# Performance work log

Hardware: AMD Instinct MI355X
Metric: run time of the kernel (lower is better)

## Reference

```python
import math
import jax, jax.numpy as jnp
import numpy as np

B, S, D, H = 8, 512, 1024, 16
DH = D // H
NEG_BIG = -1.0e30  # stands in for torch's -np.inf (exp underflows to 0 identically)


def setup_inputs() -> dict:
    key0 = jax.random.key(0)
    ks = jax.random.split(key0, 20)
    n = lambda k, shp, s=1.0: jax.random.normal(k, shp, dtype=jnp.float32) * s
    inp = {}
    inp["query"] = n(ks[0], (B, S, D))
    inp["key"] = n(ks[1], (B, S, D))
    inp["value"] = n(ks[2], (B, S, D))
    # rel has exact zeros (they get masked to -10000 before its softmax)
    inp["rel"] = jax.random.randint(ks[3], (B, S, S), 0, 3).astype(jnp.float32)
    inp["timestamp"] = n(ks[4], (B, S, S))
    inp["l1"] = jnp.float32(0.3)
    inp["l2"] = jnp.float32(0.3)
    # causal mask: True = masked (future positions)
    inp["mask"] = jnp.broadcast_to(jnp.triu(jnp.ones((S, S), dtype=bool), k=1), (B, S, S))
    inp["encode_pos"] = 0
    # three qkv projection linears (total_size -> total_size)
    w = 1.0 / math.sqrt(D)
    inp["Wq"], inp["bq"] = n(ks[5], (D, D), w), jnp.zeros((D,), jnp.float32)
    inp["Wk"], inp["bk"] = n(ks[6], (D, D), w), jnp.zeros((D,), jnp.float32)
    inp["Wv"], inp["bv"] = n(ks[7], (D, D), w), jnp.zeros((D,), jnp.float32)
    # clip_factor / guessing_factor: Linear(head_size -> 1) applied to per-head key
    wh = 1.0 / math.sqrt(DH)
    inp["Wc"], inp["bc"] = n(ks[8], (1, DH), wh), jnp.zeros((1,), jnp.float32)
    inp["Wg"], inp["bg"] = n(ks[9], (1, DH), wh), jnp.zeros((1,), jnp.float32)
    return inp


def reference(query, key, value, rel, timestamp, l1, l2, mask, encode_pos,
              Wq, bq, Wk, bk, Wv, bv, Wc, bc, Wg, bg):
    b, s, d = query.shape
    dh = Wc.shape[1]
    h = d // dh

    def proj(x, W, bias):  # [b,s,d] -> [b,h,s,dh]
        return (x @ W.T + bias).reshape(b, s, h, dh).transpose(0, 2, 1, 3)

    q = proj(query, Wq, bq)
    k = proj(key, Wk, bk)
    v = proj(value, Wv, bv)

    m4 = mask[:, None]          # [b,1,s,s] broadcast over heads
    rel4 = rel[:, None]         # [b,1,s,s]
    ts4 = timestamp[:, None]    # [b,1,s,s]

    # relative softmax: zeros masked to -10000
    rel_attn = jax.nn.softmax(jnp.where(rel4 == 0, -10000.0, rel4), axis=-1)

    # scaled dot-product scores
    scores = jnp.einsum('bhqd,bhkd->bhqk', q, k) / math.sqrt(dh)
    scores = jnp.where(m4, -1.0e9, scores)

    # clip / guessing factors from per-head key -> [b,h,s,1]
    cf = k @ Wc.T + bc
    gf = k @ Wg.T + bg
    R1 = jax.nn.sigmoid(gf - cf) + gf

    # time-decay softmax
    time_stamp = jnp.where(m4, NEG_BIG, jnp.exp(-jnp.abs(ts4)))
    Rs = time_stamp + R1  # [b,h,s,s] (R1 broadcasts over last axis, as in torch)

    prob_attn = jax.nn.softmax(scores, axis=-1)
    time_attn = jax.nn.softmax(Rs, axis=-1)
    prob_attn = (1.0 - l2) * prob_attn + l2 * time_attn
    prob_attn = (1.0 - l1) * prob_attn + l1 * rel_attn

    out = jnp.einsum('bhqk,bhkd->bhqd', prob_attn, v)
    out = out.transpose(0, 2, 1, 3).reshape(b, s, d)
    return out, prob_attn
```

## Files before the change

kernel.cpp:

```cpp
#include <hip/hip_runtime.h>
#include <math.h>

typedef __attribute__((ext_vector_type(8))) short short8;
typedef __attribute__((ext_vector_type(4))) float f32x4;

#define B_  8
#define S_  512
#define D_  1024
#define H_  16
#define DH_ 64

__device__ __forceinline__ unsigned short f2bf(float f) {
    unsigned int u = __float_as_uint(f);
    u += 0x7FFFu + ((u >> 16) & 1u);
    return (unsigned short)(u >> 16);
}
__device__ __forceinline__ float bf2f(unsigned short u) {
    return __uint_as_float(((unsigned int)u) << 16);
}
__device__ __forceinline__ void gload_lds16(const void* g, void* l) {
    __builtin_amdgcn_global_load_lds(
        (const __attribute__((address_space(1))) unsigned int*)g,
        (__attribute__((address_space(3))) unsigned int*)l, 16, 0, 0);
}

__global__ __launch_bounds__(256) void conv_bf16(
    const float* __restrict__ q, const float* __restrict__ k, const float* __restrict__ v,
    const float* __restrict__ wq, const float* __restrict__ wk, const float* __restrict__ wv,
    unsigned short* __restrict__ Abf, unsigned short* __restrict__ Wbf)
{
    const size_t NA = 1048576;
    const size_t NW = 262144;
    const size_t total = 3*NA + 3*NW;
    for (size_t i4 = (size_t)blockIdx.x*blockDim.x + threadIdx.x; i4 < total;
         i4 += (size_t)gridDim.x*blockDim.x) {
        const float* s; unsigned short* d; size_t off;
        if (i4 < 3*NA) {
            const int z = (int)(i4 / NA);
            s = (z == 0) ? q : (z == 1) ? k : v;
            off = i4 - (size_t)z*NA;
            d = Abf + (size_t)z*NA*4;
        } else {
            const size_t j = i4 - 3*NA;
            const int z = (int)(j / NW);
            s = (z == 0) ? wq : (z == 1) ? wk : wv;
            off = j - (size_t)z*NW;
            d = Wbf + (size_t)z*NW*4;
        }
        const float4 f = ((const float4*)s)[off];
        ushort4 u; u.x = f2bf(f.x); u.y = f2bf(f.y); u.z = f2bf(f.z); u.w = f2bf(f.w);
        ((ushort4*)d)[off] = u;
    }
}

__global__ __launch_bounds__(256) void qkv_gemm(
    const unsigned short* __restrict__ Abf, const unsigned short* __restrict__ Wbf,
    const float* __restrict__ bq, const float* __restrict__ bk, const float* __restrict__ bv,
    unsigned short* __restrict__ qw, unsigned short* __restrict__ kw,
    unsigned short* __restrict__ vw)
{
    __shared__ unsigned short As[128][64];
    __shared__ unsigned short Bs[128][64];

    const int bid = blockIdx.x;
    const int wid = (bid & 7) * 96 + (bid >> 3);
    const int z   = wid >> 8;
    const int rem = wid & 255;
    const int bm  = (rem >> 3) * 128;
    const int bn  = (rem & 7) * 128;

    const unsigned short* A = Abf + (size_t)z * 4194304;
    const unsigned short* W = Wbf + (size_t)z * 1048576;
    const float* bias = (z == 0) ? bq : (z == 1) ? bk : bv;
    unsigned short* outp = (z == 0) ? qw : (z == 1) ? kw : vw;
    const float scale = (z == 0) ? 0.125f : 1.0f;

    const int t = threadIdx.x, w = t >> 6, l = t & 63, lr = l & 15, lg = l >> 4;
    const int wr = (w >> 1) * 64, wc = (w & 1) * 64;

    const int srow = t >> 3;
    const int scol = 8 * ((t & 7) ^ (srow & 7));
    const unsigned short* Ast = A + (size_t)(bm + srow) * 1024 + scol;
    const unsigned short* Wst = W + (size_t)(bn + srow) * 1024 + scol;
    char* AsB = (char*)As; char* BsB = (char*)Bs;

    f32x4 acc[4][4] = {};
    for (int k0 = 0; k0 < 1024; k0 += 64) {
        __syncthreads();
        #pragma unroll
        for (int j = 0; j < 4; j++) {
            gload_lds16(Ast + (size_t)(32*j)*1024 + k0, AsB + 4096*j + t*16);
            gload_lds16(Wst + (size_t)(32*j)*1024 + k0, BsB + 4096*j + t*16);
        }
        __syncthreads();
        #pragma unroll
        for (int s = 0; s < 2; s++) {
            short8 af[4], bf4[4];
            #pragma unroll
            for (int i = 0; i < 4; i++) {
                const int row = wr + 16*i + lr;
                af[i] = *(const short8*)(AsB + row*128 + (((4*s + lg) ^ (row & 7)) << 4));
            }
            #pragma unroll
            for (int j = 0; j < 4; j++) {
                const int row = wc + 16*j + lr;
                bf4[j] = *(const short8*)(BsB + row*128 + (((4*s + lg) ^ (row & 7)) << 4));
            }
            #pragma unroll
            for (int i = 0; i < 4; i++)
                #pragma unroll
                for (int j = 0; j < 4; j++)
                    acc[i][j] = __builtin_amdgcn_mfma_f32_16x16x32_bf16(af[i], bf4[j], acc[i][j], 0, 0, 0);
        }
    }

    #pragma unroll
    for (int j = 0; j < 4; j++) {
        const int n = bn + wc + 16*j + lr;
        const float bvx = bias[n];
        const int h = n >> 6, dh = n & 63;
        #pragma unroll
        for (int i = 0; i < 4; i++)
            #pragma unroll
            for (int r = 0; r < 4; r++) {
                const int m = bm + wr + 16*i + 4*lg + r;
                const int bb = m >> 9, s = m & 511;
                outp[(((size_t)(bb*H_ + h))*S_ + s)*DH_ + dh] = f2bf((acc[i][j][r] + bvx) * scale);
            }
    }
}

__global__ __launch_bounds__(256) void vtrans(const unsigned short* __restrict__ vw,
                                              unsigned short* __restrict__ vtw)
{
    __shared__ unsigned short tile[64][68];
    const int bh = blockIdx.y, sc = blockIdx.x * 64;
    const unsigned short* src = vw + (size_t)bh * S_ * DH_;
    unsigned short* dst = vtw + (size_t)bh * DH_ * S_;
    const int t = threadIdx.x;
    const int r = t >> 4, c4 = (t & 15) << 2;
    #pragma unroll
    for (int i = 0; i < 4; i++)
        *(ushort4*)&tile[r + 16*i][c4] = *(const ushort4*)&src[(size_t)(sc + r + 16*i)*DH_ + c4];
    __syncthreads();
    const int dh = t >> 2, sg = (t & 3) * 16;
    #pragma unroll
    for (int e = 0; e < 16; e += 4) {
        ushort4 u;
        u.x = tile[sg + e + 0][dh]; u.y = tile[sg + e + 1][dh];
        u.z = tile[sg + e + 2][dh]; u.w = tile[sg + e + 3][dh];
        *(ushort4*)&dst[(size_t)dh*S_ + sc + sg + e] = u;
    }
}

__global__ __launch_bounds__(256) void e_kernel(
    const float* __restrict__ rel, const float* __restrict__ tsp,
    const float* __restrict__ pl1, const float* __restrict__ pl2,
    unsigned short* __restrict__ E)
{
    const int t = threadIdx.x, w = t >> 6, l = t & 63;
    const int ridx = blockIdx.x * 4 + w;
    const int q = ridx & (S_ - 1);
    const float l1 = *pl1, l2 = *pl2;
    const float c_t = (1.f - l1) * l2, c_r = l1;
    const float* tr = tsp + (size_t)ridx * S_;
    const float* rr = rel + (size_t)ridx * S_;

    float tv[8], rv[8]; float st = 0.f, sr = 0.f;
    #pragma unroll
    for (int j = 0; j < 8; j++) {
        const int k = l + 64*j;
        const float rvv = rr[k];
        rv[j] = (rvv != 0.f) ? __expf(rvv) : 0.f;
        sr += rv[j];
        float tvv = 0.f;
        if (k <= q) tvv = __expf(__expf(-fabsf(tr[k])));
        tv[j] = tvv; st += tvv;
    }
    #pragma unroll
    for (int m = 32; m; m >>= 1) { st += __shfl_xor(st, m); sr += __shfl_xor(sr, m); }
    const float ti   = c_t / st;
    const float riv  = (sr > 0.f) ? c_r / sr : 0.f;
    const float runi = (sr > 0.f) ? 0.f : c_r / (float)S_;

    unsigned short* Er = E + (size_t)ridx * S_;
    #pragma unroll
    for (int j = 0; j < 8; j++) {
        const int k = l + 64*j;
        Er[k] = f2bf(tv[j]*ti + rv[j]*riv + runi);
    }
}

__global__ __launch_bounds__(256) void attn_mfma(
    const unsigned short* __restrict__ qw, const unsigned short* __restrict__ kw,
    const unsigned short* __restrict__ vtw, const unsigned short* __restrict__ E,
    const float* __restrict__ pl1, const float* __restrict__ pl2,
    float* __restrict__ out, float* __restrict__ prob)
{
    __shared__ unsigned short Ps[2][64][72];

    const int t = threadIdx.x, w = t >> 6, l = t & 63, lr = l & 15, lg = l >> 4;
    const int bid = blockIdx.x;
    const int j   = bid >> 3;
    const int bh  = (bid & 7) * 16 + (j & 15);
    const int b   = bh >> 4, h = bh & 15;
    const int q0  = (j >> 4) * 64;
    const float l1 = *pl1, l2 = *pl2;
    const float c_p = (1.f - l1) * (1.f - l2);
    const unsigned short* qp = qw + (size_t)bh * (S_ * DH_);
    const unsigned short* kp = kw + (size_t)bh * (S_ * DH_);
    const unsigned short* vt = vtw + (size_t)bh * (DH_ * S_);

    short8 qa[2];
    #pragma unroll
    for (int s = 0; s < 2; s++)
        qa[s] = *(const short8*)&qp[(size_t)(q0 + 16*w + lr)*DH_ + 32*s + 8*lg];

    const int qrb = q0 + 16*w + 4*lg;

    unsigned int scp[8][4][2];
    #pragma unroll
    for (int ch = 0; ch < 8; ch++) {
        f32x4 a4[4] = {};
        #pragma unroll
        for (int s = 0; s < 2; s++)
            #pragma unroll
            for (int g = 0; g < 4; g++) {
                const short8 kb = *(const short8*)&kp[(size_t)(ch*64 + 16*g + lr)*DH_ + 32*s + 8*lg];
                a4[g] = __builtin_amdgcn_mfma_f32_16x16x32_bf16(qa[s], kb, a4[g], 0, 0, 0);
            }
        #pragma unroll
        for (int g = 0; g < 4; g++) {
            const int k = 64*ch + 16*g + lr;
            const float v0 = (k <= qrb + 0) ? a4[g][0] : -1e30f;
            const float v1 = (k <= qrb + 1) ? a4[g][1] : -1e30f;
            const float v2 = (k <= qrb + 2) ? a4[g][2] : -1e30f;
            const float v3 = (k <= qrb + 3) ? a4[g][3] : -1e30f;
            scp[ch][g][0] = ((unsigned)f2bf(v1) << 16) | f2bf(v0);
            scp[ch][g][1] = ((unsigned)f2bf(v3) << 16) | f2bf(v2);
        }
    }

    float mx[4] = {-1e30f, -1e30f, -1e30f, -1e30f};
    #pragma unroll
    for (int ch = 0; ch < 8; ch++)
        #pragma unroll
        for (int g = 0; g < 4; g++) {
            const unsigned u0 = scp[ch][g][0], u1 = scp[ch][g][1];
            mx[0] = fmaxf(mx[0], __uint_as_float(u0 << 16));
            mx[1] = fmaxf(mx[1], __uint_as_float(u0 & 0xffff0000u));
            mx[2] = fmaxf(mx[2], __uint_as_float(u1 << 16));
            mx[3] = fmaxf(mx[3], __uint_as_float(u1 & 0xffff0000u));
        }
    #pragma unroll
    for (int i = 0; i < 4; i++)
        #pragma unroll
        for (int m = 8; m; m >>= 1) mx[i] = fmaxf(mx[i], __shfl_xor(mx[i], m));

    float sm[4] = {0.f, 0.f, 0.f, 0.f};
    #pragma unroll
    for (int ch = 0; ch < 8; ch++)
        #pragma unroll
        for (int g = 0; g < 4; g++) {
            const unsigned u0 = scp[ch][g][0], u1 = scp[ch][g][1];
            const float e0 = __expf(__uint_as_float(u0 << 16)          - mx[0]);
            const float e1 = __expf(__uint_as_float(u0 & 0xffff0000u) - mx[1]);
            const float e2 = __expf(__uint_as_float(u1 << 16)          - mx[2]);
            const float e3 = __expf(__uint_as_float(u1 & 0xffff0000u) - mx[3]);
            sm[0] += e0; sm[1] += e1; sm[2] += e2; sm[3] += e3;
            scp[ch][g][0] = ((unsigned)f2bf(e1) << 16) | f2bf(e0);
            scp[ch][g][1] = ((unsigned)f2bf(e3) << 16) | f2bf(e2);
        }
    #pragma unroll
    for (int i = 0; i < 4; i++)
        #pragma unroll
        for (int m = 8; m; m >>= 1) sm[i] += __shfl_xor(sm[i], m);
    float pinv[4];
    #pragma unroll
    for (int i = 0; i < 4; i++) pinv[i] = c_p / sm[i];

    f32x4 pv[4] = {};
    const unsigned short* Eb = E + ((size_t)b * S_ + qrb) * S_;
    float* pr = prob + ((size_t)bh * S_ + qrb) * S_;
    const int prow = 16*w + 4*lg;

    #pragma unroll
    for (int ch = 0; ch < 8; ch++) {
        const int p = ch & 1;
        #pragma unroll
        for (int g = 0; g < 4; g++) {
            const int kc = 16*g + lr;
            const unsigned u0 = scp[ch][g][0], u1 = scp[ch][g][1];
            const size_t eb = (size_t)(64*ch + kc);
            const float f0 = __uint_as_float(u0 << 16)          * pinv[0] + bf2f(Eb[eb]);
            const float f1 = __uint_as_float(u0 & 0xffff0000u) * pinv[1] + bf2f(Eb[eb + 512]);
            const float f2 = __uint_as_float(u1 << 16)          * pinv[2] + bf2f(Eb[eb + 1024]);
            const float f3 = __uint_as_float(u1 & 0xffff0000u) * pinv[3] + bf2f(Eb[eb + 1536]);
            Ps[p][prow + 0][kc] = f2bf(f0);
            Ps[p][prow + 1][kc] = f2bf(f1);
            Ps[p][prow + 2][kc] = f2bf(f2);
            Ps[p][prow + 3][kc] = f2bf(f3);
            pr[eb]        = f0;
            pr[eb + 512]  = f1;
            pr[eb + 1024] = f2;
            pr[eb + 1536] = f3;
        }
        __syncthreads();
        #pragma unroll
        for (int s = 0; s < 2; s++) {
            const short8 pa = *(const short8*)&Ps[p][16*w + lr][32*s + 8*lg];
            #pragma unroll
            for (int g = 0; g < 4; g++) {
                const short8 vb = *(const short8*)&vt[(size_t)(16*g + lr)*S_ + 64*ch + 32*s + 8*lg];
                pv[g] = __builtin_amdgcn_mfma_f32_16x16x32_bf16(pa, vb, pv[g], 0, 0, 0);
            }
        }
    }

    #pragma unroll
    for (int g = 0; g < 4; g++)
        #pragma unroll
        for (int i = 0; i < 4; i++)
            out[((size_t)(b*S_ + qrb + i))*D_ + h*DH_ + 16*g + lr] = pv[g][i];
}

extern "C" void kernel_launch(void* const* d_in, const int* in_sizes, int n_in,
                              void* d_out, int out_size, void* d_ws, size_t ws_size,
                              hipStream_t stream)
{
    const float* query = (const float*)d_in[0];
    const float* key   = (const float*)d_in[1];
    const float* value = (const float*)d_in[2];
    const float* rel   = (const float*)d_in[3];
    const float* tsp   = (const float*)d_in[4];
    const float* l1    = (const float*)d_in[5];
    const float* l2    = (const float*)d_in[6];
    const float* Wq = (const float*)d_in[9];
    const float* bq = (const float*)d_in[10];
    const float* Wk = (const float*)d_in[11];
    const float* bk = (const float*)d_in[12];
    const float* Wv = (const float*)d_in[13];
    const float* bv = (const float*)d_in[14];

    float* out  = (float*)d_out;
    float* prob = (float*)d_out + (size_t)B_ * S_ * D_;

    unsigned short* Abf = (unsigned short*)prob;

    const size_t headN = (size_t)B_ * H_ * S_ * DH_;
    unsigned short* Wbf = (unsigned short*)d_ws;
    unsigned short* qw  = Wbf + 3*1048576;
    unsigned short* kw  = qw + headN;
    unsigned short* vw  = kw + headN;
    unsigned short* vtw = vw + headN;
    unsigned short* Ew  = vtw + headN;

    conv_bf16<<<2048, 256, 0, stream>>>(query, key, value, Wq, Wk, Wv, Abf, Wbf);

    qkv_gemm<<<768, 256, 0, stream>>>(Abf, Wbf, bq, bk, bv, qw, kw, vw);

    dim3 gt(8, B_ * H_);
    vtrans<<<gt, 256, 0, stream>>>(vw, vtw);

    e_kernel<<<(B_ * S_) / 4, 256, 0, stream>>>(rel, tsp, l1, l2, Ew);

    attn_mfma<<<1024, 256, 0, stream>>>(qw, kw, vtw, Ew, l1, l2, out, prob);
}
```

Measured before the change: 143.1 us.

## Fuse bf16 conversion and V transpose into QKV GEMM, use nontemporal stores

Removes the separate fp32-to-bf16 conversion kernel and the V transpose kernel. The GEMM now loads fp32 activations and weights directly, packs them to bf16 with v_cvt_pk_bf16_f32 into swizzled LDS, and writes V straight out in transposed layout. It also switches the prob and out stores to nontemporal. The cost is double the global bytes per GEMM tile load, register-staged loads in place of direct-to-LDS loads, and narrower strided stores for the V epilogue.

Measured after the change: 140.9 us. No clear change (-1.5%).

```diff
diff --git a/kernel.cpp b/kernel.cpp
--- a/kernel.cpp
+++ b/kernel.cpp
@@ -18,46 +18,18 @@
 __device__ __forceinline__ float bf2f(unsigned short u) {
     return __uint_as_float(((unsigned int)u) << 16);
 }
-__device__ __forceinline__ void gload_lds16(const void* g, void* l) {
-    __builtin_amdgcn_global_load_lds(
-        (const __attribute__((address_space(1))) unsigned int*)g,
-        (__attribute__((address_space(3))) unsigned int*)l, 16, 0, 0);
-}
-
-__global__ __launch_bounds__(256) void conv_bf16(
-    const float* __restrict__ q, const float* __restrict__ k, const float* __restrict__ v,
-    const float* __restrict__ wq, const float* __restrict__ wk, const float* __restrict__ wv,
-    unsigned short* __restrict__ Abf, unsigned short* __restrict__ Wbf)
-{
-    const size_t NA = 1048576;
-    const size_t NW = 262144;
-    const size_t total = 3*NA + 3*NW;
-    for (size_t i4 = (size_t)blockIdx.x*blockDim.x + threadIdx.x; i4 < total;
-         i4 += (size_t)gridDim.x*blockDim.x) {
-        const float* s; unsigned short* d; size_t off;
-        if (i4 < 3*NA) {
-            const int z = (int)(i4 / NA);
-            s = (z == 0) ? q : (z == 1) ? k : v;
-            off = i4 - (size_t)z*NA;
-            d = Abf + (size_t)z*NA*4;
-        } else {
-            const size_t j = i4 - 3*NA;
-            const int z = (int)(j / NW);
-            s = (z == 0) ? wq : (z == 1) ? wk : wv;
-            off = j - (size_t)z*NW;
-            d = Wbf + (size_t)z*NW*4;
-        }
-        const float4 f = ((const float4*)s)[off];
-        ushort4 u; u.x = f2bf(f.x); u.y = f2bf(f.y); u.z = f2bf(f.z); u.w = f2bf(f.w);
-        ((ushort4*)d)[off] = u;
-    }
+__device__ __forceinline__ unsigned cvtpk(float lo, float hi) {
+    unsigned r;
+    asm("v_cvt_pk_bf16_f32 %0, %1, %2" : "=v"(r) : "v"(lo), "v"(hi));
+    return r;
 }
 
 __global__ __launch_bounds__(256) void qkv_gemm(
-    const unsigned short* __restrict__ Abf, const unsigned short* __restrict__ Wbf,
+    const float* __restrict__ Aq, const float* __restrict__ Ak, const float* __restrict__ Av,
+    const float* __restrict__ Wq, const float* __restrict__ Wk, const float* __restrict__ Wv,
     const float* __restrict__ bq, const float* __restrict__ bk, const float* __restrict__ bv,
     unsigned short* __restrict__ qw, unsigned short* __restrict__ kw,
-    unsigned short* __restrict__ vw)
+    unsigned short* __restrict__ vtw)
 {
     __shared__ unsigned short As[128][64];
     __shared__ unsigned short Bs[128][64];
@@ -69,28 +41,40 @@
     const int bm  = (rem >> 3) * 128;
     const int bn  = (rem & 7) * 128;
 
-    const unsigned short* A = Abf + (size_t)z * 4194304;
-    const unsigned short* W = Wbf + (size_t)z * 1048576;
+    const float* A = (z == 0) ? Aq : (z == 1) ? Ak : Av;
+    const float* W = (z == 0) ? Wq : (z == 1) ? Wk : Wv;
     const float* bias = (z == 0) ? bq : (z == 1) ? bk : bv;
-    unsigned short* outp = (z == 0) ? qw : (z == 1) ? kw : vw;
     const float scale = (z == 0) ? 0.125f : 1.0f;
 
     const int t = threadIdx.x, w = t >> 6, l = t & 63, lr = l & 15, lg = l >> 4;
     const int wr = (w >> 1) * 64, wc = (w & 1) * 64;
 
     const int srow = t >> 3;
-    const int scol = 8 * ((t & 7) ^ (srow & 7));
-    const unsigned short* Ast = A + (size_t)(bm + srow) * 1024 + scol;
-    const unsigned short* Wst = W + (size_t)(bn + srow) * 1024 + scol;
+    const int sblk = t & 7;
     char* AsB = (char*)As; char* BsB = (char*)Bs;
 
     f32x4 acc[4][4] = {};
     for (int k0 = 0; k0 < 1024; k0 += 64) {
         __syncthreads();
+        float4 av[4][2], wv4[4][2];
         #pragma unroll
         for (int j = 0; j < 4; j++) {
-            gload_lds16(Ast + (size_t)(32*j)*1024 + k0, AsB + 4096*j + t*16);
-            gload_lds16(Wst + (size_t)(32*j)*1024 + k0, BsB + 4096*j + t*16);
+            const float* ap = A + (size_t)(bm + 32*j + srow)*1024 + k0 + sblk*8;
+            const float* wp = W + (size_t)(bn + 32*j + srow)*1024 + k0 + sblk*8;
+            av[j][0]  = ((const float4*)ap)[0]; av[j][1]  = ((const float4*)ap)[1];
+            wv4[j][0] = ((const float4*)wp)[0]; wv4[j][1] = ((const float4*)wp)[1];
+        }
+        #pragma unroll
+        for (int j = 0; j < 4; j++) {
+            const int row = 32*j + srow;
+            const int byte = row*128 + ((sblk ^ (row & 7)) << 4);
+            uint4 ua, uw;
+            ua.x = cvtpk(av[j][0].x, av[j][0].y);  ua.y = cvtpk(av[j][0].z, av[j][0].w);
+            ua.z = cvtpk(av[j][1].x, av[j][1].y);  ua.w = cvtpk(av[j][1].z, av[j][1].w);
+            uw.x = cvtpk(wv4[j][0].x, wv4[j][0].y); uw.y = cvtpk(wv4[j][0].z, wv4[j][0].w);
+            uw.z = cvtpk(wv4[j][1].x, wv4[j][1].y); uw.w = cvtpk(wv4[j][1].z, wv4[j][1].w);
+            *(uint4*)(AsB + byte) = ua;
+            *(uint4*)(BsB + byte) = uw;
         }
         __syncthreads();
         #pragma unroll
@@ -114,42 +98,38 @@
         }
     }
 
-    #pragma unroll
-    for (int j = 0; j < 4; j++) {
-        const int n = bn + wc + 16*j + lr;
-        const float bvx = bias[n];
-        const int h = n >> 6, dh = n & 63;
-        #pragma unroll
-        for (int i = 0; i < 4; i++)
-            #pragma unroll
-            for (int r = 0; r < 4; r++) {
-                const int m = bm + wr + 16*i + 4*lg + r;
-                const int bb = m >> 9, s = m & 511;
-                outp[(((size_t)(bb*H_ + h))*S_ + s)*DH_ + dh] = f2bf((acc[i][j][r] + bvx) * scale);
-            }
-    }
-}
-
-__global__ __launch_bounds__(256) void vtrans(const unsigned short* __restrict__ vw,
-                                              unsigned short* __restrict__ vtw)
-{
-    __shared__ unsigned short tile[64][68];
-    const int bh = blockIdx.y, sc = blockIdx.x * 64;
-    const unsigned short* src = vw + (size_t)bh * S_ * DH_;
-    unsigned short* dst = vtw + (size_t)bh * DH_ * S_;
-    const int t = threadIdx.x;
-    const int r = t >> 4, c4 = (t & 15) << 2;
-    #pragma unroll
-    for (int i = 0; i < 4; i++)
-        *(ushort4*)&tile[r + 16*i][c4] = *(const ushort4*)&src[(size_t)(sc + r + 16*i)*DH_ + c4];
-    __syncthreads();
-    const int dh = t >> 2, sg = (t & 3) * 16;
-    #pragma unroll
-    for (int e = 0; e < 16; e += 4) {
-        ushort4 u;
-        u.x = tile[sg + e + 0][dh]; u.y = tile[sg + e + 1][dh];
-        u.z = tile[sg + e + 2][dh]; u.w = tile[sg + e + 3][dh];
-        *(ushort4*)&dst[(size_t)dh*S_ + sc + sg + e] = u;
+    if (z < 2) {
+        unsigned short* outp = (z == 0) ? qw : kw;
+        #pragma unroll
+        for (int j = 0; j < 4; j++) {
+            const int n = bn + wc + 16*j + lr;
+            const float bvx = bias[n];
+            const int h = n >> 6, dh = n & 63;
+            #pragma unroll
+            for (int i = 0; i < 4; i++)
+                #pragma unroll
+                for (int r = 0; r < 4; r++) {
+                    const int m = bm + wr + 16*i + 4*lg + r;
+                    const int bb = m >> 9, s = m & 511;
+                    outp[(((size_t)(bb*H_ + h))*S_ + s)*DH_ + dh] = f2bf((acc[i][j][r] + bvx) * scale);
+                }
+        }
+    } else {
+        #pragma unroll
+        for (int j = 0; j < 4; j++) {
+            const int n = bn + wc + 16*j + lr;
+            const float bvx = bias[n];
+            const int h = n >> 6, dh = n & 63;
+            #pragma unroll
+            for (int i = 0; i < 4; i++) {
+                const int m0 = bm + wr + 16*i + 4*lg;
+                const int bb = m0 >> 9, s0 = m0 & 511;
+                ushort4 u;
+                u.x = f2bf(acc[i][j][0] + bvx); u.y = f2bf(acc[i][j][1] + bvx);
+                u.z = f2bf(acc[i][j][2] + bvx); u.w = f2bf(acc[i][j][3] + bvx);
+                *(ushort4*)&vtw[(((size_t)(bb*H_ + h))*DH_ + dh)*S_ + s0] = u;
+            }
+        }
     }
 }
 
@@ -300,10 +280,10 @@
             Ps[p][prow + 1][kc] = f2bf(f1);
             Ps[p][prow + 2][kc] = f2bf(f2);
             Ps[p][prow + 3][kc] = f2bf(f3);
-            pr[eb]        = f0;
-            pr[eb + 512]  = f1;
-            pr[eb + 1024] = f2;
-            pr[eb + 1536] = f3;
+            __builtin_nontemporal_store(f0, &pr[eb]);
+            __builtin_nontemporal_store(f1, &pr[eb + 512]);
+            __builtin_nontemporal_store(f2, &pr[eb + 1024]);
+            __builtin_nontemporal_store(f3, &pr[eb + 1536]);
         }
         __syncthreads();
         #pragma unroll
@@ -321,7 +301,8 @@
     for (int g = 0; g < 4; g++)
         #pragma unroll
         for (int i = 0; i < 4; i++)
-            out[((size_t)(b*S_ + qrb + i))*D_ + h*DH_ + 16*g + lr] = pv[g][i];
+            __builtin_nontemporal_store(pv[g][i],
+                &out[((size_t)(b*S_ + qrb + i))*D_ + h*DH_ + 16*g + lr]);
 }
 
 extern "C" void kernel_launch(void* const* d_in, const int* in_sizes, int n_in,
@@ -345,22 +326,14 @@
     float* out  = (float*)d_out;
     float* prob = (float*)d_out + (size_t)B_ * S_ * D_;
 
-    unsigned short* Abf = (unsigned short*)prob;
-
     const size_t headN = (size_t)B_ * H_ * S_ * DH_;
-    unsigned short* Wbf = (unsigned short*)d_ws;
-    unsigned short* qw  = Wbf + 3*1048576;
+    unsigned short* qw  = (unsigned short*)d_ws;
     unsigned short* kw  = qw + headN;
-    unsigned short* vw  = kw + headN;
-    unsigned short* vtw = vw + headN;
+    unsigned short* vtw = kw + headN;
     unsigned short* Ew  = vtw + headN;
 
-    conv_bf16<<<2048, 256, 0, stream>>>(query, key, value, Wq, Wk, Wv, Abf, Wbf);
-
-    qkv_gemm<<<768, 256, 0, stream>>>(Abf, Wbf, bq, bk, bv, qw, kw, vw);
-
-    dim3 gt(8, B_ * H_);
-    vtrans<<<gt, 256, 0, stream>>>(vw, vtw);
+    qkv_gemm<<<768, 256, 0, stream>>>(query, key, value, Wq, Wk, Wv,
+                                      bq, bk, bv, qw, kw, vtw);
 
     e_kernel<<<(B_ * S_) / 4, 256, 0, stream>>>(rel, tsp, l1, l2, Ew);
 
```
